# Kernel tuning notes

Measured on AMD Instinct MI355X. Metric: run time of the kernel, lower is better.

Reference implementation:

```python
import jax, jax.numpy as jnp
import numpy as np

BZ, N, NH, HD = 256, 360, 4, 8  # batch, roi_num, num_heads, head_dim
POOL_L = int(N * 0.7)  # 252


def _lrelu(x):
    return jax.nn.leaky_relu(x, 0.2)


def _bn(x, g, b):
    # training-mode BatchNorm1d over flattened (bz*roi) dim, biased variance, eps=1e-5
    mu = x.mean(0)
    var = x.var(0)
    return (x - mu) * jax.lax.rsqrt(var + 1e-5) * g + b


def setup_inputs() -> dict:
    key = jax.random.key(0)
    ks = jax.random.split(key, 20)
    def rn(i, shape, s=0.05):
        return jax.random.normal(ks[i], shape, dtype=jnp.float32) * s
    z = lambda *s: jnp.zeros(s, jnp.float32)
    o = lambda *s: jnp.ones(s, jnp.float32)
    return {
        "m": jax.random.normal(ks[0], (BZ, N, N), dtype=jnp.float32),
        "node_feature": jax.random.normal(ks[1], (BZ, N, N), dtype=jnp.float32),
        "cls": rn(2, (1, 16)),
        "gcn0_w": rn(3, (N, N)), "gcn0_b": z(N),
        "gcn1_w": rn(4, (N, N)), "gcn1_b": z(N),
        "gcn2_w1": rn(5, (N, 64)), "gcn2_b1": z(64),
        "gcn2_w2": rn(6, (64, 16)), "gcn2_b2": z(16),
        "sc_w": rn(7, (N, 16)), "sc_b": z(16),
        "bn0_g": o(N), "bn0_b": z(N),
        "bn1_g": o(N), "bn1_b": z(N),
        "bn2_g": o(16), "bn2_b": z(16),
        "wq": rn(8, (16, NH * HD)), "bq": z(NH * HD),
        "wk": rn(9, (16, NH * HD)), "bk": z(NH * HD),
        "wv": rn(10, (16, NH * HD)), "bv": z(NH * HD),
        "wo": rn(11, (NH * HD, 16)), "bo": z(16),
        "f1_w": rn(12, (16, 64)), "f1_b": z(64),
        "f2_w": rn(13, (64, 32)), "f2_b": z(32),
        "f3_w": rn(14, (32, 2)), "f3_b": z(2),
    }


def reference(m, node_feature, cls, gcn0_w, gcn0_b, gcn1_w, gcn1_b,
              gcn2_w1, gcn2_b1, gcn2_w2, gcn2_b2, sc_w, sc_b,
              bn0_g, bn0_b, bn1_g, bn1_b, bn2_g, bn2_b,
              wq, bq, wk, bk, wv, bv, wo, bo,
              f1_w, f1_b, f2_w, f2_b, f3_w, f3_b):
    bz, n = m.shape[0], m.shape[1]
    # einsum('ijk,ijp->ijp', m, x) == rowsum(m) * x (elementwise), faithful to source
    rowsum = m.sum(-1, keepdims=True)  # [bz, n, 1]

    x_clone = jnp.zeros_like(node_feature)
    x = node_feature
    # layer 0
    x = rowsum * x
    x = _lrelu(x @ gcn0_w + gcn0_b) + x_clone
    x = _bn(x.reshape(bz * n, -1), bn0_g, bn0_b).reshape(bz, n, -1)
    x_clone = x
    # layer 1
    x = rowsum * x
    x = _lrelu(x @ gcn1_w + gcn1_b) + x_clone
    x = _bn(x.reshape(bz * n, -1), bn1_g, bn1_b).reshape(bz, n, -1)
    x_clone = x
    # layer 2 (with shortcut projection)
    x = rowsum * x
    h = _lrelu(_lrelu(x @ gcn2_w1 + gcn2_b1) @ gcn2_w2 + gcn2_b2)
    x = h + _lrelu(x_clone @ sc_w + sc_b)
    x = _bn(x.reshape(bz * n, -1), bn2_g, bn2_b).reshape(bz, n, 16)

    # prepend cls token (vectorized, replaces the per-sample python loop)
    x_in = jnp.concatenate([jnp.broadcast_to(cls, (bz, 1, 16)), x], axis=1)  # [bz, n+1, 16]

    # Encoder: multi-head self-attention
    q = (x_in @ wq + bq).reshape(bz, n + 1, NH, HD)
    k = (x_in @ wk + bk).reshape(bz, n + 1, NH, HD)
    v = (x_in @ wv + bv).reshape(bz, n + 1, NH, HD)
    scale = 1.0 / jnp.sqrt(jnp.asarray(HD, jnp.float32))
    attn = jax.nn.softmax(jnp.einsum('bqhd,bkhd->bhqk', q, k) * scale, axis=-1)  # [bz,4,n+1,n+1]
    out = jnp.einsum('bhqk,bkhd->bqhd', attn, v).reshape(bz, n + 1, NH * HD) @ wo + bo  # [bz,n+1,16]

    # cls-row attention summed over 4 heads, drop cls column
    score = attn[:, :, 0, :].sum(1)[:, 1:]  # [bz, n]
    sc = score
    vals, idx = jax.lax.top_k(score, POOL_L)  # top-l sort/gather
    w = jax.nn.softmax(vals, axis=-1)  # [bz, l]
    x_body = out[:, 1:, :]  # [bz, n, 16]
    x_p = jnp.take_along_axis(x_body, idx[:, :, None], axis=1)  # [bz, l, 16]
    pooled = jnp.einsum('bl,bld->bd', w, x_p)  # [bz, 16]

    h = _lrelu(pooled @ f1_w + f1_b)
    h = _lrelu(h @ f2_w + f2_b)
    logits = h @ f3_w + f3_b  # [bz, 2]
    return (logits, jax.nn.sigmoid(sc), attn)
```

## Files before the change

kernel.cpp:

```cpp
#include <hip/hip_runtime.h>
#include <math.h>

#define BZ 256
#define NN 360
#define NP1 361
#define MROWS (BZ*NN)
#define POOLL 252
#define KP 384

typedef __attribute__((ext_vector_type(8))) short bf16x8;
typedef __attribute__((ext_vector_type(4))) float f32x4;

__device__ __forceinline__ float lrelu(float x){ return x > 0.f ? x : 0.2f*x; }

__device__ __forceinline__ ushort f2bf(float f){
    union { float f; uint u; } v; v.f = f;
    uint u = v.u + 0x7FFFu + ((v.u >> 16) & 1u);
    return (ushort)(u >> 16);
}
__device__ __forceinline__ float bf2f(ushort h){
    union { uint u; float f; } v; v.u = ((uint)h) << 16;
    return v.f;
}
__device__ __forceinline__ void split2(float v, ushort& hi, ushort& lo){
    hi = f2bf(v);
    lo = f2bf(v - bf2f(hi));
}

__device__ __forceinline__ void gload16(const void* g, void* l){
    __builtin_amdgcn_global_load_lds((const __attribute__((address_space(1))) uint*)g,
                                     (__attribute__((address_space(3))) uint*)l, 16, 0, 0);
}

__device__ __forceinline__ void stage_plane(const ushort* __restrict__ src, size_t srow0,
                                            ushort (*P)[32], int k0, int t){
    int w = t >> 6;
    #pragma unroll
    for (int i=0;i<2;i++){
        int u = i*256 + t;
        int row = u >> 2, ccs = u & 3;
        int cg = ccs ^ ((row >> 1) & 3);
        const ushort* g = src + (srow0 + row)*KP + k0 + cg*8;
        char* l = (char*)P + i*4096 + w*1024;
        gload16(g, l);
    }
}

__device__ __forceinline__ bf16x8 frag_read(const ushort (*P)[32], int row, int g){
    return *(const bf16x8*)((const char*)P + row*64 + ((g ^ ((row >> 1) & 3)) * 16));
}

__global__ void k_zero(float* p, int n){
    int i = blockIdx.x*blockDim.x + threadIdx.x;
    if (i < n) p[i] = 0.f;
}

__global__ __launch_bounds__(256)
void k_rowsum(const float* __restrict__ m, float* __restrict__ rowsum){
    int wid = (blockIdx.x*blockDim.x + threadIdx.x) >> 6;
    int lane = threadIdx.x & 63;
    if (wid >= MROWS) return;
    const float4* p = (const float4*)(m + (size_t)wid*NN);
    float s = 0.f;
    {
        float4 f = p[lane];
        s += f.x + f.y + f.z + f.w;
    }
    if (lane < 26){
        float4 f = p[64 + lane];
        s += f.x + f.y + f.z + f.w;
    }
    #pragma unroll
    for (int off = 32; off; off >>= 1) s += __shfl_down(s, off);
    if (lane == 0) rowsum[wid] = s;
}

__global__ __launch_bounds__(384)
void k_prepw(const float* __restrict__ W, int ncols, int joff,
             const float* __restrict__ s, const float* __restrict__ h,
             ushort* __restrict__ Wth, ushort* __restrict__ Wtl, float* __restrict__ cvec)
{
    int j = blockIdx.x;
    int k = threadIdx.x;
    __shared__ float red[6];
    float wv = 0.f, hv = 0.f, sv = 1.f;
    if (k < NN && j < ncols){
        wv = W[(size_t)k*ncols + j];
        if (s) sv = s[k];
        if (h) hv = h[k];
    }
    ushort hi, lo; split2(wv * sv, hi, lo);
    Wth[(size_t)(joff + j)*KP + k] = hi;
    Wtl[(size_t)(joff + j)*KP + k] = lo;
    float v = hv * wv;
    #pragma unroll
    for (int off = 32; off; off >>= 1) v += __shfl_down(v, off);
    int lane = k & 63, wid = k >> 6;
    if (lane == 0) red[wid] = v;
    __syncthreads();
    if (k == 0) cvec[joff + j] = red[0]+red[1]+red[2]+red[3]+red[4]+red[5];
}

template<bool AF32, bool RESID>
__global__ __launch_bounds__(256)
void k_gemm_mfma(const void* __restrict__ Avh, const ushort* __restrict__ Avl,
                 const ushort* __restrict__ Wth, const ushort* __restrict__ Wtl,
                 const float* __restrict__ cvec, const float* __restrict__ bias,
                 const float* __restrict__ rowsum,
                 const float* __restrict__ bns, const float* __restrict__ bnh,
                 ushort* __restrict__ Yhi, ushort* __restrict__ Ylo,
                 float* __restrict__ colsum, float* __restrict__ colsq)
{
    __shared__ ushort Ah[128][32];
    __shared__ ushort Al[128][32];
    __shared__ ushort Bh[128][32];
    __shared__ ushort Bl[128][32];
    int t = threadIdx.x;
    int w = t >> 6, lane = t & 63;
    int l15 = lane & 15, g = lane >> 4;
    int idx = blockIdx.x;
    int gr = idx & 7;
    int rem = idx >> 3;
    int jcb = rem % 3;
    int gq = rem / 3;
    int rowblk = (gq*8 + gr) * 128;
    int colblk = jcb * 128;

    f32x4 acc[2][8];
    #pragma unroll
    for (int i=0;i<2;i++)
        #pragma unroll
        for (int j=0;j<8;j++)
            #pragma unroll
            for (int e=0;e<4;e++) acc[i][j][e] = 0.f;

    for (int kt = 0; kt < 12; ++kt){
        int k0 = kt * 32;
        if (AF32){
            const float* A = (const float*)Avh;
            int row = t >> 1, half = t & 1;
            int fr = (row >> 1) & 3;
            #pragma unroll
            for (int c=0;c<2;c++){
                int cg = half*2 + c;
                int k = k0 + cg*8;
                float4 f0 = make_float4(0.f,0.f,0.f,0.f);
                float4 f1 = make_float4(0.f,0.f,0.f,0.f);
                if (k < NN){
                    f0 = *(const float4*)&A[(size_t)(rowblk+row)*NN + k];
                    f1 = *(const float4*)&A[(size_t)(rowblk+row)*NN + k + 4];
                }
                ushort h0,l0,h1,l1,h2,l2,h3,l3,h4,l4,h5,l5,h6,l6,h7,l7;
                split2(f0.x,h0,l0); split2(f0.y,h1,l1); split2(f0.z,h2,l2); split2(f0.w,h3,l3);
                split2(f1.x,h4,l4); split2(f1.y,h5,l5); split2(f1.z,h6,l6); split2(f1.w,h7,l7);
                uint4 hv = make_uint4((uint)h0|((uint)h1<<16), (uint)h2|((uint)h3<<16),
                                      (uint)h4|((uint)h5<<16), (uint)h6|((uint)h7<<16));
                uint4 lv = make_uint4((uint)l0|((uint)l1<<16), (uint)l2|((uint)l3<<16),
                                      (uint)l4|((uint)l5<<16), (uint)l6|((uint)l7<<16));
                int ccs = cg ^ fr;
                *(uint4*)((char*)Ah + row*64 + ccs*16) = hv;
                *(uint4*)((char*)Al + row*64 + ccs*16) = lv;
            }
        } else {
            stage_plane((const ushort*)Avh, (size_t)rowblk, Ah, k0, t);
            stage_plane(Avl,               (size_t)rowblk, Al, k0, t);
        }
        stage_plane(Wth, (size_t)colblk, Bh, k0, t);
        stage_plane(Wtl, (size_t)colblk, Bl, k0, t);
        __syncthreads();

        bf16x8 ah0 = frag_read(Ah, 32*w + l15, g);
        bf16x8 ah1 = frag_read(Ah, 32*w + 16 + l15, g);
        bf16x8 al0 = frag_read(Al, 32*w + l15, g);
        bf16x8 al1 = frag_read(Al, 32*w + 16 + l15, g);
        #pragma unroll
        for (int nj=0;nj<8;nj++){
            bf16x8 bh = frag_read(Bh, 16*nj + l15, g);
            bf16x8 bl = frag_read(Bl, 16*nj + l15, g);
            acc[0][nj] = __builtin_amdgcn_mfma_f32_16x16x32_bf16(ah0, bh, acc[0][nj], 0, 0, 0);
            acc[0][nj] = __builtin_amdgcn_mfma_f32_16x16x32_bf16(al0, bh, acc[0][nj], 0, 0, 0);
            acc[0][nj] = __builtin_amdgcn_mfma_f32_16x16x32_bf16(ah0, bl, acc[0][nj], 0, 0, 0);
            acc[1][nj] = __builtin_amdgcn_mfma_f32_16x16x32_bf16(ah1, bh, acc[1][nj], 0, 0, 0);
            acc[1][nj] = __builtin_amdgcn_mfma_f32_16x16x32_bf16(al1, bh, acc[1][nj], 0, 0, 0);
            acc[1][nj] = __builtin_amdgcn_mfma_f32_16x16x32_bf16(ah1, bl, acc[1][nj], 0, 0, 0);
        }
        __syncthreads();
    }

    const ushort* AHg = (const ushort*)Avh;
    float cs_part[8] = {0,0,0,0,0,0,0,0}, cq_part[8] = {0,0,0,0,0,0,0,0};
    #pragma unroll
    for (int mi=0;mi<2;mi++){
        #pragma unroll
        for (int nj=0;nj<8;nj++){
            f32x4 d = acc[mi][nj];
            #pragma unroll
            for (int r=0;r<4;r++){
                int row = rowblk + 32*w + 16*mi + 4*g + r;
                int col = colblk + 16*nj + l15;
                float v = 0.f;
                if (col < NN){
                    float pre = rowsum[row] * (d[r] + cvec[col]) + bias[col];
                    v = lrelu(pre);
                    if (RESID){
                        size_t ai = (size_t)row*KP + col;
                        float ar = bf2f(AHg[ai]) + bf2f(Avl[ai]);
                        v += ar * bns[col] + bnh[col];
                    }
                }
                ushort hi, lo; split2(v, hi, lo);
                Yhi[(size_t)row*KP + col] = hi;
                Ylo[(size_t)row*KP + col] = lo;
                cs_part[nj] += v;
                cq_part[nj] += v*v;
            }
        }
    }
    #pragma unroll
    for (int nj=0;nj<8;nj++){
        cs_part[nj] += __shfl_xor(cs_part[nj], 16); cs_part[nj] += __shfl_xor(cs_part[nj], 32);
        cq_part[nj] += __shfl_xor(cq_part[nj], 16); cq_part[nj] += __shfl_xor(cq_part[nj], 32);
    }
    float* red = (float*)&Ah[0][0];
    if (lane < 16){
        #pragma unroll
        for (int nj=0;nj<8;nj++) red[w*128 + nj*16 + l15] = cs_part[nj];
    }
    __syncthreads();
    if (t < 128 && colblk + t < NN)
        atomicAdd(&colsum[colblk + t], red[t] + red[128+t] + red[256+t] + red[384+t]);
    __syncthreads();
    if (lane < 16){
        #pragma unroll
        for (int nj=0;nj<8;nj++) red[w*128 + nj*16 + l15] = cq_part[nj];
    }
    __syncthreads();
    if (t < 128 && colblk + t < NN)
        atomicAdd(&colsq[colblk + t], red[t] + red[128+t] + red[256+t] + red[384+t]);
}

__global__ void k_bnfin(const float* __restrict__ colsum, const float* __restrict__ colsq,
                        const float* __restrict__ g, const float* __restrict__ b, int ncols,
                        float* __restrict__ scale, float* __restrict__ shift){
    int j = blockIdx.x*blockDim.x + threadIdx.x;
    if (j >= ncols) return;
    float mu = colsum[j] / (float)MROWS;
    float var = colsq[j] / (float)MROWS - mu*mu;
    float sc = g[j] * rsqrtf(var + 1e-5f);
    scale[j] = sc;
    shift[j] = b[j] - mu*sc;
}

__global__ __launch_bounds__(256)
void k_gemm2_mfma(const ushort* __restrict__ AH, const ushort* __restrict__ AL,
                  const ushort* __restrict__ Wth, const ushort* __restrict__ Wtl,
                  const float* __restrict__ cvec, const float* __restrict__ b1,
                  const float* __restrict__ scb, const float* __restrict__ rowsum,
                  float* __restrict__ h1buf, float* __restrict__ scbuf)
{
    __shared__ ushort Ah[128][32];
    __shared__ ushort Al[128][32];
    __shared__ ushort Bh[80][40];
    __shared__ ushort Bl[80][40];
    int t = threadIdx.x;
    int w = t >> 6, lane = t & 63;
    int l15 = lane & 15, g = lane >> 4;
    int rowblk = blockIdx.x * 128;

    f32x4 acc[2][5];
    #pragma unroll
    for (int i=0;i<2;i++)
        #pragma unroll
        for (int j=0;j<5;j++)
            #pragma unroll
            for (int e=0;e<4;e++) acc[i][j][e] = 0.f;

    for (int kt = 0; kt < 12; ++kt){
        int k0 = kt * 32;
        stage_plane(AH, (size_t)rowblk, Ah, k0, t);
        stage_plane(AL, (size_t)rowblk, Al, k0, t);
        #pragma unroll
        for (int l=0;l<2;l++){
            int c = t + l*256;
            if (c < 320){
                int col = c >> 2, kk = (c & 3)*8;
                ((int4*)&Bh[col][kk])[0] = *(const int4*)&Wth[(size_t)col*KP + k0 + kk];
                ((int4*)&Bl[col][kk])[0] = *(const int4*)&Wtl[(size_t)col*KP + k0 + kk];
            }
        }
        __syncthreads();
        bf16x8 ah0 = frag_read(Ah, 32*w + l15, g);
        bf16x8 ah1 = frag_read(Ah, 32*w + 16 + l15, g);
        bf16x8 al0 = frag_read(Al, 32*w + l15, g);
        bf16x8 al1 = frag_read(Al, 32*w + 16 + l15, g);
        #pragma unroll
        for (int nj=0;nj<5;nj++){
            bf16x8 bh = *(const bf16x8*)&Bh[16*nj + l15][8*g];
            bf16x8 bl = *(const bf16x8*)&Bl[16*nj + l15][8*g];
            acc[0][nj] = __builtin_amdgcn_mfma_f32_16x16x32_bf16(ah0, bh, acc[0][nj], 0, 0, 0);
            acc[0][nj] = __builtin_amdgcn_mfma_f32_16x16x32_bf16(al0, bh, acc[0][nj], 0, 0, 0);
            acc[0][nj] = __builtin_amdgcn_mfma_f32_16x16x32_bf16(ah0, bl, acc[0][nj], 0, 0, 0);
            acc[1][nj] = __builtin_amdgcn_mfma_f32_16x16x32_bf16(ah1, bh, acc[1][nj], 0, 0, 0);
            acc[1][nj] = __builtin_amdgcn_mfma_f32_16x16x32_bf16(al1, bh, acc[1][nj], 0, 0, 0);
            acc[1][nj] = __builtin_amdgcn_mfma_f32_16x16x32_bf16(ah1, bl, acc[1][nj], 0, 0, 0);
        }
        __syncthreads();
    }

    #pragma unroll
    for (int mi=0;mi<2;mi++){
        #pragma unroll
        for (int nj=0;nj<5;nj++){
            f32x4 d = acc[mi][nj];
            #pragma unroll
            for (int r=0;r<4;r++){
                int row = rowblk + 32*w + 16*mi + 4*g + r;
                int col = 16*nj + l15;
                if (nj < 4){
                    float pre = rowsum[row] * (d[r] + cvec[col]) + b1[col];
                    h1buf[(size_t)row*64 + col] = lrelu(pre);
                } else {
                    int cc = col - 64;
                    float pre = d[r] + cvec[col] + scb[cc];
                    scbuf[(size_t)row*16 + cc] = lrelu(pre);
                }
            }
        }
    }
}

__global__ __launch_bounds__(256)
void k_stage2(const float* __restrict__ h1buf, const float* __restrict__ scbuf,
              const float* __restrict__ w2, const float* __restrict__ b2,
              float* __restrict__ x2, float* __restrict__ colsum, float* __restrict__ colsq)
{
    __shared__ float Hs[64][65];
    __shared__ float Ws[64][17];
    __shared__ float red[16][16];
    int t = threadIdx.x;
    int rowblk = blockIdx.x * 64;
    #pragma unroll
    for (int l=0;l<4;l++){
        int idx = t + l*256;
        Ws[idx>>4][idx&15] = w2[idx];
    }
    #pragma unroll
    for (int l=0;l<16;l++){
        int idx = t + l*256;
        Hs[idx>>6][idx&63] = h1buf[(size_t)rowblk*64 + idx];
    }
    __syncthreads();
    int col = t & 15, rb = t >> 4;
    float ps=0.f, pq=0.f;
    #pragma unroll
    for (int gg=0; gg<4; gg++){
        int r = rb + gg*16;
        float s = b2[col];
        #pragma unroll
        for (int c=0;c<64;c++) s += Hs[r][c]*Ws[c][col];
        float v = lrelu(s) + scbuf[(size_t)(rowblk+r)*16 + col];
        x2[(size_t)(rowblk+r)*16 + col] = v;
        ps += v; pq += v*v;
    }
    red[rb][col] = ps; __syncthreads();
    if (t < 16){
        float s=0.f;
        for (int g=0; g<16; g++) s += red[g][t];
        atomicAdd(&colsum[t], s);
    }
    __syncthreads();
    red[rb][col] = pq; __syncthreads();
    if (t < 16){
        float s=0.f;
        for (int g=0; g<16; g++) s += red[g][t];
        atomicAdd(&colsq[t], s);
    }
}

__device__ __forceinline__ float bfly8(float o[8], int lane){
    int b0 = lane & 1, b1 = lane & 2, b2 = lane & 4;
    float n[4];
    #pragma unroll
    for (int j=0;j<4;j++){
        float give = b0 ? o[j] : o[j+4];
        float keep = b0 ? o[j+4] : o[j];
        n[j] = keep + __shfl_xor(give, 1);
    }
    float m2[2];
    #pragma unroll
    for (int j=0;j<2;j++){
        float give = b1 ? n[j] : n[j+2];
        float keep = b1 ? n[j+2] : n[j];
        m2[j] = keep + __shfl_xor(give, 2);
    }
    float give = b2 ? m2[0] : m2[1];
    float keep = b2 ? m2[1] : m2[0];
    float v = keep + __shfl_xor(give, 4);
    v += __shfl_xor(v, 8);
    v += __shfl_xor(v, 16);
    v += __shfl_xor(v, 32);
    return v;
}

__global__ __launch_bounds__(256)
void k_attn(const float* __restrict__ x2, const float* __restrict__ s2, const float* __restrict__ h2,
            const float* __restrict__ cls,
            const float* __restrict__ wq, const float* __restrict__ bq,
            const float* __restrict__ wk, const float* __restrict__ bk,
            const float* __restrict__ wv, const float* __restrict__ bv,
            float* __restrict__ attn, float* __restrict__ obuf)
{
    int blk = blockIdx.x;
    int chunk = blk & 1;
    int bh = blk >> 1;
    int b = bh >> 2, h = bh & 3;
    __shared__ float4 KV[4][NP1];
    int t = threadIdx.x;

    for (int task = t; task < NP1*16; task += 256){
        int r = task >> 4;
        int sub = task & 15;
        int tensor = sub >> 3;
        int d = sub & 7;
        float x[16];
        if (r == 0){
            #pragma unroll
            for (int c=0;c<16;c++) x[c] = cls[c];
        } else {
            const float4* xr = (const float4*)&x2[((size_t)b*NN + (r-1))*16];
            #pragma unroll
            for (int c4=0;c4<4;c4++){
                float4 f = xr[c4];
                x[c4*4+0] = f.x*s2[c4*4+0] + h2[c4*4+0];
                x[c4*4+1] = f.y*s2[c4*4+1] + h2[c4*4+1];
                x[c4*4+2] = f.z*s2[c4*4+2] + h2[c4*4+2];
                x[c4*4+3] = f.w*s2[c4*4+3] + h2[c4*4+3];
            }
        }
        const float* W  = tensor ? wv : wk;
        const float* Bb = tensor ? bv : bk;
        float a = Bb[h*8+d];
        #pragma unroll
        for (int c=0;c<16;c++) a += x[c]*W[c*32 + h*8 + d];
        ((float*)&KV[tensor*2 + (d>>2)][r])[d&3] = a;
    }
    __syncthreads();

    int w = t >> 6, lane = t & 63;
    float kreg[6][8], vreg[6][8];
    #pragma unroll
    for (int j=0;j<6;j++){
        int ki = lane + (j<<6);
        int kc = ki > 360 ? 360 : ki;
        float4 ka = KV[0][kc], kb = KV[1][kc];
        float4 va = KV[2][kc], vb = KV[3][kc];
        kreg[j][0]=ka.x; kreg[j][1]=ka.y; kreg[j][2]=ka.z; kreg[j][3]=ka.w;
        kreg[j][4]=kb.x; kreg[j][5]=kb.y; kreg[j][6]=kb.z; kreg[j][7]=kb.w;
        vreg[j][0]=va.x; vreg[j][1]=va.y; vreg[j][2]=va.z; vreg[j][3]=va.w;
        vreg[j][4]=vb.x; vreg[j][5]=vb.y; vreg[j][6]=vb.z; vreg[j][7]=vb.w;
    }

    int row_half = lane >> 5;
    int l5 = lane & 31;
    int qd = l5 & 7, qkc = (l5 >> 3);
    int cbase = chunk * 181;
    int cend  = chunk ? NP1 : 181;

    for (int qi0 = cbase + (w<<1); qi0 < cend; qi0 += 8){
        int qi1 = qi0 + 1;
        bool v1 = (qi1 < cend);

        int myrow = row_half ? (v1 ? qi1 : qi0) : qi0;
        float part = 0.f;
        {
            float xv[4];
            if (myrow == 0){
                #pragma unroll
                for (int c=0;c<4;c++) xv[c] = cls[qkc*4+c];
            } else {
                float4 f = *(const float4*)&x2[((size_t)b*NN + (myrow-1))*16 + qkc*4];
                xv[0] = f.x*s2[qkc*4+0] + h2[qkc*4+0];
                xv[1] = f.y*s2[qkc*4+1] + h2[qkc*4+1];
                xv[2] = f.z*s2[qkc*4+2] + h2[qkc*4+2];
                xv[3] = f.w*s2[qkc*4+3] + h2[qkc*4+3];
            }
            #pragma unroll
            for (int c=0;c<4;c++)
                part += xv[c] * wq[(qkc*4+c)*32 + h*8 + qd];
        }
        part += __shfl_xor(part, 8);
        part += __shfl_xor(part, 16);
        part = (part + bq[h*8+qd]) * 0.35355339059327373f;
        float q0[8], q1[8];
        #pragma unroll
        for (int d=0;d<8;d++){ q0[d] = __shfl(part, d); q1[d] = __shfl(part, 32+d); }

        float e0[6], e1[6];
        float mx0 = -1e30f, mx1 = -1e30f;
        #pragma unroll
        for (int j=0;j<6;j++){
            int ki = lane + (j<<6);
            float s0 = 0.f, s1 = 0.f;
            #pragma unroll
            for (int d=0;d<8;d++){ s0 += q0[d]*kreg[j][d]; s1 += q1[d]*kreg[j][d]; }
            if (ki >= NP1){ s0 = -1e30f; s1 = -1e30f; }
            e0[j] = s0; e1[j] = s1;
            mx0 = fmaxf(mx0, s0); mx1 = fmaxf(mx1, s1);
        }
        #pragma unroll
        for (int off=32; off; off>>=1){
            mx0 = fmaxf(mx0, __shfl_xor(mx0, off));
            mx1 = fmaxf(mx1, __shfl_xor(mx1, off));
        }
        float sum0 = 0.f, sum1 = 0.f;
        #pragma unroll
        for (int j=0;j<6;j++){
            float p0 = __expf(e0[j]-mx0);
            float p1 = __expf(e1[j]-mx1);
            e0[j]=p0; e1[j]=p1;
            sum0 += p0; sum1 += p1;
        }
        #pragma unroll
        for (int off=32; off; off>>=1){
            sum0 += __shfl_xor(sum0, off);
            sum1 += __shfl_xor(sum1, off);
        }
        float inv0 = 1.f/sum0;
        float inv1 = 1.f/sum1;

        size_t abase = (size_t)bh*NP1*NP1 + (size_t)qi0*NP1;
        float o0[8] = {0,0,0,0,0,0,0,0};
        float o1[8] = {0,0,0,0,0,0,0,0};
        #pragma unroll
        for (int j=0;j<6;j++){
            int ki = lane + (j<<6);
            float p0 = e0[j]*inv0;
            float p1 = e1[j]*inv1;
            if (ki < NP1){
                attn[abase + ki] = p0;
                if (v1) attn[abase + NP1 + ki] = p1;
            }
            #pragma unroll
            for (int d=0;d<8;d++){
                o0[d] += p0*vreg[j][d];
                o1[d] += p1*vreg[j][d];
            }
        }
        float val0 = bfly8(o0, lane);
        float val1 = bfly8(o1, lane);
        int l7 = lane & 7;
        int dmap = ((l7&1)<<2) | (l7&2) | ((l7>>2)&1);
        if (lane < 8)
            obuf[((size_t)b*NP1 + qi0)*32 + h*8 + dmap] = val0;
        else if (lane < 16 && v1)
            obuf[((size_t)b*NP1 + qi1)*32 + h*8 + dmap] = val1;
    }
}

__global__ void k_score(const float* __restrict__ attn, float* __restrict__ out_sig,
                        float* __restrict__ score_raw){
    int b = blockIdx.x;
    for (int j = threadIdx.x; j < NN; j += blockDim.x){
        float s = 0.f;
        #pragma unroll
        for (int h=0; h<4; h++)
            s += attn[(((size_t)b*4+h)*NP1)*NP1 + 1 + j];
        score_raw[b*NN + j] = s;
        out_sig[b*NN + j] = 1.f/(1.f + __expf(-s));
    }
}

__global__ __launch_bounds__(256)
void k_pool(const float* __restrict__ score_raw, const float* __restrict__ obuf,
            const float* __restrict__ wo, const float* __restrict__ bo,
            const float* __restrict__ f1w, const float* __restrict__ f1b,
            const float* __restrict__ f2w, const float* __restrict__ f2b,
            const float* __restrict__ f3w, const float* __restrict__ f3b,
            float* __restrict__ logits)
{
    int b = blockIdx.x;
    __shared__ float sc[NN];
    __shared__ float w[NN];
    __shared__ float red[256];
    __shared__ float pooled32[32];
    __shared__ float p16[16];
    __shared__ float h64[64];
    __shared__ float h32[32];
    int t = threadIdx.x;
    for (int i=t; i<NN; i+=256) sc[i] = score_raw[b*NN+i];
    __syncthreads();
    float mx = -1e30f;
    for (int i=t; i<NN; i+=256) mx = fmaxf(mx, sc[i]);
    red[t] = mx; __syncthreads();
    for (int s=128; s; s>>=1){ if (t<s) red[t]=fmaxf(red[t],red[t+s]); __syncthreads(); }
    mx = red[0];
    __syncthreads();
    float psum = 0.f;
    for (int i=t; i<NN; i+=256){
        float si = sc[i];
        int r = 0;
        for (int j=0;j<NN;j++){
            float sj = sc[j];
            r += (sj > si) || (sj == si && j < i);
        }
        float wi = (r < POOLL) ? __expf(si - mx) : 0.f;
        w[i] = wi;
        psum += wi;
    }
    red[t] = psum; __syncthreads();
    for (int s=128; s; s>>=1){ if (t<s) red[t]+=red[t+s]; __syncthreads(); }
    float inv = 1.f / red[0];
    __syncthreads();
    if (t < 32){
        float s = 0.f;
        for (int i=0;i<NN;i++) s += w[i] * obuf[((size_t)b*NP1 + 1 + i)*32 + t];
        pooled32[t] = s * inv;
    }
    __syncthreads();
    if (t < 16){
        float s = bo[t];
        for (int d=0;d<32;d++) s += pooled32[d]*wo[d*16+t];
        p16[t] = s;
    }
    __syncthreads();
    if (t < 64){
        float s = f1b[t];
        for (int c=0;c<16;c++) s += p16[c]*f1w[c*64+t];
        h64[t] = lrelu(s);
    }
    __syncthreads();
    if (t < 32){
        float s = f2b[t];
        for (int c=0;c<64;c++) s += h64[c]*f2w[c*32+t];
        h32[t] = lrelu(s);
    }
    __syncthreads();
    if (t < 2){
        float s = f3b[t];
        for (int c=0;c<32;c++) s += h32[c]*f3w[c*2+t];
        logits[b*2+t] = s;
    }
}

extern "C" void kernel_launch(void* const* d_in, const int* in_sizes, int n_in,
                              void* d_out, int out_size, void* d_ws, size_t ws_size,
                              hipStream_t stream)
{
    const float* m    = (const float*)d_in[0];
    const float* nf   = (const float*)d_in[1];
    const float* cls  = (const float*)d_in[2];
    const float* g0w  = (const float*)d_in[3];
    const float* g0b  = (const float*)d_in[4];
    const float* g1w  = (const float*)d_in[5];
    const float* g1b  = (const float*)d_in[6];
    const float* g2w1 = (const float*)d_in[7];
    const float* g2b1 = (const float*)d_in[8];
    const float* g2w2 = (const float*)d_in[9];
    const float* g2b2 = (const float*)d_in[10];
    const float* scw  = (const float*)d_in[11];
    const float* scb  = (const float*)d_in[12];
    const float* bn0g = (const float*)d_in[13];
    const float* bn0b = (const float*)d_in[14];
    const float* bn1g = (const float*)d_in[15];
    const float* bn1b = (const float*)d_in[16];
    const float* bn2g = (const float*)d_in[17];
    const float* bn2b = (const float*)d_in[18];
    const float* wq = (const float*)d_in[19];
    const float* bq = (const float*)d_in[20];
    const float* wk = (const float*)d_in[21];
    const float* bk = (const float*)d_in[22];
    const float* wv = (const float*)d_in[23];
    const float* bv = (const float*)d_in[24];
    const float* wo = (const float*)d_in[25];
    const float* bo = (const float*)d_in[26];
    const float* f1w = (const float*)d_in[27];
    const float* f1b = (const float*)d_in[28];
    const float* f2w = (const float*)d_in[29];
    const float* f2b = (const float*)d_in[30];
    const float* f3w = (const float*)d_in[31];
    const float* f3b = (const float*)d_in[32];

    float* out_logits = (float*)d_out;
    float* out_sig = out_logits + 512;
    float* attn = out_sig + (size_t)BZ*NN;

    char* base = (char*)attn;
    const size_t szy = (size_t)MROWS * KP * 2;
    ushort* y0h = (ushort*)base;
    ushort* y0l = (ushort*)(base + szy);
    ushort* y1h = (ushort*)(base + 2*szy);
    ushort* y1l = (ushort*)(base + 3*szy);
    float*  h1buf = (float*)(base + 4*szy);
    const size_t szh = (size_t)MROWS * 64 * 4;
    float*  scbuf = (float*)(base + 4*szy + szh);
    const size_t szsc = (size_t)MROWS * 16 * 4;
    ushort* Wt0h = (ushort*)(base + 4*szy + szh + szsc);
    ushort* Wt0l = Wt0h + (size_t)KP*KP;
    ushort* Wt1h = Wt0l + (size_t)KP*KP;
    ushort* Wt1l = Wt1h + (size_t)KP*KP;
    ushort* Wt2h = Wt1l + (size_t)KP*KP;
    ushort* Wt2l = Wt2h + (size_t)KP*KP;
    float*  c0  = (float*)(Wt2l + (size_t)KP*KP);
    float*  c1  = c0 + KP;
    float*  c2  = c1 + KP;

    float* ws = (float*)d_ws;
    float* rowsum = ws;                ws += MROWS;
    float* stats  = ws;                ws += 1472;
    float* cs0 = stats, *cq0 = stats+360, *cs1 = stats+720, *cq1 = stats+1080,
         * cs2 = stats+1440, *cq2 = stats+1456;
    float* s0 = ws;  ws += 360;
    float* h0 = ws;  ws += 360;
    float* s1 = ws;  ws += 360;
    float* hh1 = ws; ws += 360;
    float* s2 = ws;  ws += 16;
    float* h2 = ws;  ws += 16;
    float* x2 = ws;       ws += (size_t)MROWS*16;
    float* obuf = ws;     ws += (size_t)BZ*NP1*32;
    float* score_raw = ws; ws += (size_t)BZ*NN;

    k_zero<<<6, 256, 0, stream>>>(stats, 1472);
    k_rowsum<<<MROWS/4, 256, 0, stream>>>(m, rowsum);
    k_prepw<<<KP, KP, 0, stream>>>(g0w, 360, 0, nullptr, nullptr, Wt0h, Wt0l, c0);

    k_gemm_mfma<true,false><<<2160, 256, 0, stream>>>(nf, nullptr, Wt0h, Wt0l, c0, g0b, rowsum, nullptr, nullptr, y0h, y0l, cs0, cq0);
    k_bnfin<<<1, 384, 0, stream>>>(cs0, cq0, bn0g, bn0b, 360, s0, h0);
    k_prepw<<<KP, KP, 0, stream>>>(g1w, 360, 0, s0, h0, Wt1h, Wt1l, c1);
    k_gemm_mfma<false,true><<<2160, 256, 0, stream>>>(y0h, y0l, Wt1h, Wt1l, c1, g1b, rowsum, s0, h0, y1h, y1l, cs1, cq1);
    k_bnfin<<<1, 384, 0, stream>>>(cs1, cq1, bn1g, bn1b, 360, s1, hh1);
    k_prepw<<<64, KP, 0, stream>>>(g2w1, 64, 0, s1, hh1, Wt2h, Wt2l, c2);
    k_prepw<<<16, KP, 0, stream>>>(scw, 16, 64, s1, hh1, Wt2h, Wt2l, c2);
    k_gemm2_mfma<<<720, 256, 0, stream>>>(y1h, y1l, Wt2h, Wt2l, c2, g2b1, scb, rowsum, h1buf, scbuf);
    k_stage2<<<1440, 256, 0, stream>>>(h1buf, scbuf, g2w2, g2b2, x2, cs2, cq2);
    k_bnfin<<<1, 64, 0, stream>>>(cs2, cq2, bn2g, bn2b, 16, s2, h2);
    k_attn<<<BZ*4*2, 256, 0, stream>>>(x2, s2, h2, cls, wq, bq, wk, bk, wv, bv, attn, obuf);
    k_score<<<BZ, 256, 0, stream>>>(attn, out_sig, score_raw);
    k_pool<<<BZ, 256, 0, stream>>>(score_raw, obuf, wo, bo, f1w, f1b, f2w, f2b, f3w, f3b, out_logits);
}
```

Before: 752.0 us.

## Precompute QKV in separate kernel and fuse score into pooling kernel

Adds a per-batch k_qkv kernel that computes the Q, K and V projections once and stores them in a workspace buffer. Before this, each of the 8 attention blocks per batch rebuilt K/V for its head and chunk, with the two chunks duplicating the same work, and Q was computed inside the loop using shuffles. k_attn now just loads the precomputed Q/K/V into shared memory. The k_score kernel is folded into k_pool to save a launch and a round trip through score_raw, at the cost of an extra qkv buffer write and read.

```diff
diff --git a/kernel.cpp b/kernel.cpp
--- a/kernel.cpp
+++ b/kernel.cpp
@@ -377,6 +377,60 @@
     }
 }
 
+__global__ __launch_bounds__(256)
+void k_qkv(const float* __restrict__ x2, const float* __restrict__ s2, const float* __restrict__ h2,
+           const float* __restrict__ cls,
+           const float* __restrict__ wq, const float* __restrict__ bq,
+           const float* __restrict__ wk, const float* __restrict__ bk,
+           const float* __restrict__ wv, const float* __restrict__ bv,
+           float* __restrict__ qkv)
+{
+    int b = blockIdx.x;
+    __shared__ float4 xin[NP1][4];
+    int t = threadIdx.x;
+    for (int i = t; i < NP1*4; i += 256){
+        int r = i >> 2, c4 = i & 3;
+        float4 f;
+        if (r == 0) f = ((const float4*)cls)[c4];
+        else {
+            f = *(const float4*)&x2[((size_t)b*NN + r-1)*16 + c4*4];
+            f.x = f.x*s2[c4*4+0] + h2[c4*4+0];
+            f.y = f.y*s2[c4*4+1] + h2[c4*4+1];
+            f.z = f.z*s2[c4*4+2] + h2[c4*4+2];
+            f.w = f.w*s2[c4*4+3] + h2[c4*4+3];
+        }
+        xin[r][c4] = f;
+    }
+    __syncthreads();
+    for (int task = t; task < 3*NP1*8; task += 256){
+        int tn = task / (NP1*8);
+        int rem = task - tn*(NP1*8);
+        int r = rem >> 3, d4 = rem & 7;
+        const float* W  = (tn==0) ? wq : ((tn==1) ? wk : wv);
+        const float* Bb = (tn==0) ? bq : ((tn==1) ? bk : bv);
+        float o0 = Bb[d4*4+0], o1 = Bb[d4*4+1], o2 = Bb[d4*4+2], o3 = Bb[d4*4+3];
+        #pragma unroll
+        for (int c4=0;c4<4;c4++){
+            float4 xf = xin[r][c4];
+            float xs[4] = {xf.x, xf.y, xf.z, xf.w};
+            #pragma unroll
+            for (int cc=0;cc<4;cc++){
+                int c = c4*4 + cc;
+                float x = xs[cc];
+                o0 += x * W[c*32 + d4*4 + 0];
+                o1 += x * W[c*32 + d4*4 + 1];
+                o2 += x * W[c*32 + d4*4 + 2];
+                o3 += x * W[c*32 + d4*4 + 3];
+            }
+        }
+        if (tn == 0){
+            const float sc = 0.35355339059327373f;
+            o0 *= sc; o1 *= sc; o2 *= sc; o3 *= sc;
+        }
+        *(float4*)&qkv[(((size_t)b*3 + tn)*NP1 + r)*32 + d4*4] = make_float4(o0,o1,o2,o3);
+    }
+}
+
 __device__ __forceinline__ float bfly8(float o[8], int lane){
     int b0 = lane & 1, b1 = lane & 2, b2 = lane & 4;
     float n[4];
@@ -403,46 +457,25 @@
 }
 
 __global__ __launch_bounds__(256)
-void k_attn(const float* __restrict__ x2, const float* __restrict__ s2, const float* __restrict__ h2,
-            const float* __restrict__ cls,
-            const float* __restrict__ wq, const float* __restrict__ bq,
-            const float* __restrict__ wk, const float* __restrict__ bk,
-            const float* __restrict__ wv, const float* __restrict__ bv,
-            float* __restrict__ attn, float* __restrict__ obuf)
+void k_attn(const float* __restrict__ qkv, float* __restrict__ attn, float* __restrict__ obuf)
 {
     int blk = blockIdx.x;
     int chunk = blk & 1;
     int bh = blk >> 1;
     int b = bh >> 2, h = bh & 3;
     __shared__ float4 KV[4][NP1];
+    __shared__ float4 QS[2][NP1];
     int t = threadIdx.x;
 
-    for (int task = t; task < NP1*16; task += 256){
-        int r = task >> 4;
-        int sub = task & 15;
-        int tensor = sub >> 3;
-        int d = sub & 7;
-        float x[16];
-        if (r == 0){
-            #pragma unroll
-            for (int c=0;c<16;c++) x[c] = cls[c];
-        } else {
-            const float4* xr = (const float4*)&x2[((size_t)b*NN + (r-1))*16];
-            #pragma unroll
-            for (int c4=0;c4<4;c4++){
-                float4 f = xr[c4];
-                x[c4*4+0] = f.x*s2[c4*4+0] + h2[c4*4+0];
-                x[c4*4+1] = f.y*s2[c4*4+1] + h2[c4*4+1];
-                x[c4*4+2] = f.z*s2[c4*4+2] + h2[c4*4+2];
-                x[c4*4+3] = f.w*s2[c4*4+3] + h2[c4*4+3];
-            }
-        }
-        const float* W  = tensor ? wv : wk;
-        const float* Bb = tensor ? bv : bk;
-        float a = Bb[h*8+d];
-        #pragma unroll
-        for (int c=0;c<16;c++) a += x[c]*W[c*32 + h*8 + d];
-        ((float*)&KV[tensor*2 + (d>>2)][r])[d&3] = a;
+    const float* qb = qkv + ((size_t)b*3 + 0)*NP1*32 + h*8;
+    const float* kb = qkv + ((size_t)b*3 + 1)*NP1*32 + h*8;
+    const float* vb = qkv + ((size_t)b*3 + 2)*NP1*32 + h*8;
+    for (int i = t; i < NP1*6; i += 256){
+        int r = i / 6, s = i - 6*(i/6);
+        int dq = s & 1;
+        if (s < 2)      QS[dq][r]   = *(const float4*)&qb[(size_t)r*32 + dq*4];
+        else if (s < 4) KV[dq][r]   = *(const float4*)&kb[(size_t)r*32 + dq*4];
+        else            KV[2+dq][r] = *(const float4*)&vb[(size_t)r*32 + dq*4];
     }
     __syncthreads();
 
@@ -452,17 +485,14 @@
     for (int j=0;j<6;j++){
         int ki = lane + (j<<6);
         int kc = ki > 360 ? 360 : ki;
-        float4 ka = KV[0][kc], kb = KV[1][kc];
-        float4 va = KV[2][kc], vb = KV[3][kc];
+        float4 ka = KV[0][kc], kb2 = KV[1][kc];
+        float4 va = KV[2][kc], vb2 = KV[3][kc];
         kreg[j][0]=ka.x; kreg[j][1]=ka.y; kreg[j][2]=ka.z; kreg[j][3]=ka.w;
-        kreg[j][4]=kb.x; kreg[j][5]=kb.y; kreg[j][6]=kb.z; kreg[j][7]=kb.w;
+        kreg[j][4]=kb2.x; kreg[j][5]=kb2.y; kreg[j][6]=kb2.z; kreg[j][7]=kb2.w;
         vreg[j][0]=va.x; vreg[j][1]=va.y; vreg[j][2]=va.z; vreg[j][3]=va.w;
-        vreg[j][4]=vb.x; vreg[j][5]=vb.y; vreg[j][6]=vb.z; vreg[j][7]=vb.w;
-    }
-
-    int row_half = lane >> 5;
-    int l5 = lane & 31;
-    int qd = l5 & 7, qkc = (l5 >> 3);
+        vreg[j][4]=vb2.x; vreg[j][5]=vb2.y; vreg[j][6]=vb2.z; vreg[j][7]=vb2.w;
+    }
+
     int cbase = chunk * 181;
     int cend  = chunk ? NP1 : 181;
 
@@ -470,30 +500,13 @@
         int qi1 = qi0 + 1;
         bool v1 = (qi1 < cend);
 
-        int myrow = row_half ? (v1 ? qi1 : qi0) : qi0;
-        float part = 0.f;
+        float q0[8], q1[8];
         {
-            float xv[4];
-            if (myrow == 0){
-                #pragma unroll
-                for (int c=0;c<4;c++) xv[c] = cls[qkc*4+c];
-            } else {
-                float4 f = *(const float4*)&x2[((size_t)b*NN + (myrow-1))*16 + qkc*4];
-                xv[0] = f.x*s2[qkc*4+0] + h2[qkc*4+0];
-                xv[1] = f.y*s2[qkc*4+1] + h2[qkc*4+1];
-                xv[2] = f.z*s2[qkc*4+2] + h2[qkc*4+2];
-                xv[3] = f.w*s2[qkc*4+3] + h2[qkc*4+3];
-            }
-            #pragma unroll
-            for (int c=0;c<4;c++)
-                part += xv[c] * wq[(qkc*4+c)*32 + h*8 + qd];
-        }
-        part += __shfl_xor(part, 8);
-        part += __shfl_xor(part, 16);
-        part = (part + bq[h*8+qd]) * 0.35355339059327373f;
-        float q0[8], q1[8];
-        #pragma unroll
-        for (int d=0;d<8;d++){ q0[d] = __shfl(part, d); q1[d] = __shfl(part, 32+d); }
+            float4 a = QS[0][qi0], c = QS[1][qi0];
+            q0[0]=a.x;q0[1]=a.y;q0[2]=a.z;q0[3]=a.w;q0[4]=c.x;q0[5]=c.y;q0[6]=c.z;q0[7]=c.w;
+            float4 a1 = QS[0][qi1], c1 = QS[1][qi1];
+            q1[0]=a1.x;q1[1]=a1.y;q1[2]=a1.z;q1[3]=a1.w;q1[4]=c1.x;q1[5]=c1.y;q1[6]=c1.z;q1[7]=c1.w;
+        }
 
         float e0[6], e1[6];
         float mx0 = -1e30f, mx1 = -1e30f;
@@ -557,26 +570,13 @@
     }
 }
 
-__global__ void k_score(const float* __restrict__ attn, float* __restrict__ out_sig,
-                        float* __restrict__ score_raw){
-    int b = blockIdx.x;
-    for (int j = threadIdx.x; j < NN; j += blockDim.x){
-        float s = 0.f;
-        #pragma unroll
-        for (int h=0; h<4; h++)
-            s += attn[(((size_t)b*4+h)*NP1)*NP1 + 1 + j];
-        score_raw[b*NN + j] = s;
-        out_sig[b*NN + j] = 1.f/(1.f + __expf(-s));
-    }
-}
-
 __global__ __launch_bounds__(256)
-void k_pool(const float* __restrict__ score_raw, const float* __restrict__ obuf,
+void k_pool(const float* __restrict__ attn, const float* __restrict__ obuf,
             const float* __restrict__ wo, const float* __restrict__ bo,
             const float* __restrict__ f1w, const float* __restrict__ f1b,
             const float* __restrict__ f2w, const float* __restrict__ f2b,
             const float* __restrict__ f3w, const float* __restrict__ f3b,
-            float* __restrict__ logits)
+            float* __restrict__ out_sig, float* __restrict__ logits)
 {
     int b = blockIdx.x;
     __shared__ float sc[NN];
@@ -587,7 +587,14 @@
     __shared__ float h64[64];
     __shared__ float h32[32];
     int t = threadIdx.x;
-    for (int i=t; i<NN; i+=256) sc[i] = score_raw[b*NN+i];
+    for (int i=t; i<NN; i+=256){
+        float s = 0.f;
+        #pragma unroll
+        for (int h=0; h<4; h++)
+            s += attn[(((size_t)b*4+h)*NP1)*NP1 + 1 + i];
+        sc[i] = s;
+        out_sig[b*NN + i] = 1.f/(1.f + __expf(-s));
+    }
     __syncthreads();
     float mx = -1e30f;
     for (int i=t; i<NN; i+=256) mx = fmaxf(mx, sc[i]);
@@ -717,7 +724,7 @@
     float* h2 = ws;  ws += 16;
     float* x2 = ws;       ws += (size_t)MROWS*16;
     float* obuf = ws;     ws += (size_t)BZ*NP1*32;
-    float* score_raw = ws; ws += (size_t)BZ*NN;
+    float* qkv = ws;      ws += (size_t)BZ*3*NP1*32;
 
     k_zero<<<6, 256, 0, stream>>>(stats, 1472);
     k_rowsum<<<MROWS/4, 256, 0, stream>>>(m, rowsum);
@@ -733,7 +740,7 @@
     k_gemm2_mfma<<<720, 256, 0, stream>>>(y1h, y1l, Wt2h, Wt2l, c2, g2b1, scb, rowsum, h1buf, scbuf);
     k_stage2<<<1440, 256, 0, stream>>>(h1buf, scbuf, g2w2, g2b2, x2, cs2, cq2);
     k_bnfin<<<1, 64, 0, stream>>>(cs2, cq2, bn2g, bn2b, 16, s2, h2);
-    k_attn<<<BZ*4*2, 256, 0, stream>>>(x2, s2, h2, cls, wq, bq, wk, bk, wv, bv, attn, obuf);
-    k_score<<<BZ, 256, 0, stream>>>(attn, out_sig, score_raw);
-    k_pool<<<BZ, 256, 0, stream>>>(score_raw, obuf, wo, bo, f1w, f1b, f2w, f2b, f3w, f3b, out_logits);
-}
+    k_qkv<<<BZ, 256, 0, stream>>>(x2, s2, h2, cls, wq, bq, wk, bk, wv, bv, qkv);
+    k_attn<<<BZ*4*2, 256, 0, stream>>>(qkv, attn, obuf);
+    k_pool<<<BZ, 256, 0, stream>>>(attn, obuf, wo, bo, f1w, f1b, f2w, f2b, f3w, f3b, out_sig, out_logits);
+}
```

Measured after the change: 742.0 us. No clear change (-1.3%).
